# Optimization experiments

Measured on AMD Instinct MI355X. Metric: run time of the kernel, lower is better.

## Reference

```python
import jax, jax.numpy as jnp
import numpy as np

B, T, H, W = 4096, 15, 28, 28
F1, F3 = 500, 10
# conv1 firing threshold from the original: 15 * (28*28 / (5*5)) * 0.35 * 0.16
CONV1_T = 15.0 * (28.0 * 28.0 / 25.0) * 0.35 * 0.16  # = 26.3424


def setup_inputs() -> dict:
    key = jax.random.key(0)
    k_in, k_w1, k_w3 = jax.random.split(key, 3)
    # Intensity-to-latency cumulative spike encoding (SpykeTorch style):
    # a pixel with intensity u fires at timestep ~ (1-u)*T and stays on
    # (spike trains are cumulative over the time dimension).
    u = jax.random.uniform(k_in, (B, 1, 1, H, W))
    t = jnp.arange(T, dtype=jnp.float32).reshape(1, T, 1, 1, 1)
    inp = (u * T <= (t + 1.0)).astype(jnp.float32)  # [B,T,1,H,W], binary, cumulative in t
    # snn.Convolution initializes weights as N(mean=0.8, std=0.05)
    w1 = 0.8 + 0.05 * jax.random.normal(k_w1, (F1, 1, H, W), dtype=jnp.float32)
    w3 = 0.8 + 0.05 * jax.random.normal(k_w3, (F3, F1), dtype=jnp.float32)
    return {"input": inp, "w1": w1, "w3": w3, "max_layer": 3}


def reference(input, w1, w3, max_layer):
    # --- conv1: kernel spans the full 28x28 field -> output spatial dims 1x1,
    # so the convolution is exactly a per-timestep GEMM (spatial dims squeezed).
    pot1 = jnp.einsum('btchw,fchw->btf', input, w1)          # [B,T,F1]
    # sf.fire(pot, CONV1_T, True): zero sub-threshold potentials, spikes = sign
    thr1 = jnp.where(pot1 >= CONV1_T, pot1, 0.0)
    spk1 = jnp.sign(thr1)
    if max_layer == 1:
        return spk1, thr1

    # --- conv3: 1x1 conv 500 -> 10 (spatial dims remain 1x1)
    pot3 = jnp.einsum('btf,gf->btg', spk1, w3)               # [B,T,F3]
    # sf.fire(pot) with threshold=None: keep only the last timestep, spikes = sign
    last = (jnp.arange(T) == T - 1).astype(pot3.dtype)[None, :, None]
    spk3 = jnp.sign(pot3 * last)                             # [B,T,F3]

    # --- sf.get_k_winners(pot3, k=1, r=0, spk3), vectorized over batch:
    # earliest spike time per feature (T - #spikes, clamped to T-1)
    first_t = jnp.clip(T - spk3.sum(axis=1), 0, T - 1).astype(jnp.int32)  # [B,F3]
    vals = jnp.take_along_axis(pot3, first_t[:, None, :], axis=1)         # [B,1,F3]
    trunc = spk3 * vals                                                   # [B,T,F3]
    v = trunc.max(axis=(1, 2), keepdims=True) * T   # large earliness bonus factor
    trunc = trunc + spk3 * v
    total = trunc.sum(axis=1)                                             # [B,F3]
    win = jnp.argmax(total, axis=1).astype(jnp.int32)
    # if no spike at all, original returns -1; decision_map is identity over 10
    out_cls = jnp.where(total.max(axis=1) != 0.0, win, -1)                # [B]
    return spk1, thr1, pot3, out_cls
```

## Files before the change

kernel.cpp:

```cpp
#include <hip/hip_runtime.h>
#include <hip/hip_bf16.h>
#include <stdint.h>


typedef _Float16     f16x8 __attribute__((ext_vector_type(8)));
typedef float        f32x4 __attribute__((ext_vector_type(4)));
typedef unsigned int u32x4 __attribute__((ext_vector_type(4)));

typedef __attribute__((address_space(3))) char        lds_char_t;
typedef const __attribute__((address_space(1))) char  gbl_char_t;

#define GLL16(gsrc, ldst) \
  __builtin_amdgcn_global_load_lds((gbl_char_t*)(gsrc), (lds_char_t*)(ldst), 16, 0, 0)

#define CONV1_T 26.3424f
#define KDIM 784
#define F1   500

__global__ __launch_bounds__(256)
void k_t0(const float* __restrict__ inp, unsigned int* __restrict__ t0nib)
{
    const int gid = blockIdx.x * 256 + threadIdx.x;
    const int b   = gid / 100;
    const int p8  = gid % 100;
    if (p8 >= 98) { t0nib[gid] = 0xFFFFFFFFu; return; }

    const float* base = inp + (size_t)b * 11760 + p8 * 8;
    float cnt[8];
    #pragma unroll
    for (int e = 0; e < 8; ++e) cnt[e] = 0.f;
    #pragma unroll
    for (int t = 0; t < 15; ++t) {
        const f32x4 v0 = *(const f32x4*)(base + t * 784);
        const f32x4 v1 = *(const f32x4*)(base + t * 784 + 4);
        #pragma unroll
        for (int e = 0; e < 4; ++e) { cnt[e] += v0[e]; cnt[e + 4] += v1[e]; }
    }
    unsigned int d = 0;
    #pragma unroll
    for (int e = 0; e < 8; ++e) {
        const unsigned int t0 = 15u - (unsigned int)cnt[e];
        d |= (t0 & 15u) << (4 * e);
    }
    t0nib[gid] = d;
}

__device__ __forceinline__
f16x8 rebuild_a(unsigned int d, int t)
{
    u32x4 br;
    #pragma unroll
    for (int h = 0; h < 4; ++h) {
        const unsigned int n0 = (d >> (8 * h))     & 15u;
        const unsigned int n1 = (d >> (8 * h + 4)) & 15u;
        br[h] = (n0 <= (unsigned)t ? 0x3C00u     : 0u)
              | (n1 <= (unsigned)t ? 0x3C000000u : 0u);
    }
    return __builtin_bit_cast(f16x8, br);
}

__global__ __launch_bounds__(256)
void k_prep(const float* __restrict__ w1, float* __restrict__ scratch)
{
    const int c = blockIdx.x * 256 + threadIdx.x;
    const int tile  = c >> 11;
    const int chunk = c & 2047;
    const int nb   = tile / 25;
    const int ks   = tile % 25;
    const int part = chunk >> 10;
    const int nl   = (chunk & 1023) >> 2;
    const int slot = chunk & 3;
    const int j    = slot ^ ((nl >> 1) & 3);
    const int k0   = ks * 32 + j * 8;
    const int ng   = nb * 256 + nl;

    f16x8 v;
    #pragma unroll
    for (int e = 0; e < 8; ++e) {
        const int kk = k0 + e;
        const float val = (ng < F1 && kk < KDIM) ? w1[ng * KDIM + kk] : 0.f;
        const _Float16 h = (_Float16)val;
        v[e] = part ? (_Float16)(val - (float)h) : h;
    }
    *(f16x8*)((char*)scratch + (size_t)c * 16) = v;
}

__global__ __launch_bounds__(512, 4)
void k_conv1_t0(const unsigned char* __restrict__ t0nib,
                const float* __restrict__ bsplit,
                float* __restrict__ spk1, float* __restrict__ thr1)
{
    __shared__ _Float16 sA[2][128 * 32];
    __shared__ _Float16 sB[2][2 * 256 * 32];

    const int tid  = threadIdx.x;
    const int lane = tid & 63;
    const int wid  = tid >> 6;
    const int wm   = wid >> 2;
    const int wn   = wid & 3;
    const int lr   = lane & 15;
    const int kg   = lane >> 4;

    const int bx   = blockIdx.x;
    const int nb   = (bx >> 3) & 1;
    const int mblk = ((bx >> 4) << 3) | (bx & 7);
    const long long rowBase = (long long)mblk * 128;

    const int sm  = tid >> 2;
    const int sk8 = tid & 3;
    const int aWr = sm * 32 + (sk8 ^ ((sm >> 1) & 3)) * 8;
    const long long am = rowBase + sm;
    const int at = (int)(am % 15);
    const unsigned char* atp = t0nib + (am / 15) * 400 + sk8 * 4;

    const char* gBsrc = (const char*)bsplit + (size_t)(nb * 25) * 32768
                      + (size_t)wid * 4096 + (size_t)lane * 16;

    f32x4 acc[4][4];
    #pragma unroll
    for (int i = 0; i < 4; ++i)
        #pragma unroll
        for (int j = 0; j < 4; ++j) acc[i][j] = {0.f, 0.f, 0.f, 0.f};

    int aOff[4], bOff[4];
    #pragma unroll
    for (int fm = 0; fm < 4; ++fm) {
        const int r = wm * 64 + fm * 16 + lr;
        aOff[fm] = r * 32 + (kg ^ ((r >> 1) & 3)) * 8;
    }
    #pragma unroll
    for (int fn = 0; fn < 4; ++fn) {
        const int n = wn * 64 + fn * 16 + lr;
        bOff[fn] = n * 32 + (kg ^ ((n >> 1) & 3)) * 8;
    }

    {
        #pragma unroll
        for (int i = 0; i < 4; ++i)
            GLL16(gBsrc + i * 1024, (lds_char_t*)&sB[0][0] + wid * 4096 + i * 1024);
        const unsigned int d = *(const unsigned int*)(atp);
        *(f16x8*)&sA[0][aWr] = rebuild_a(d, at);
    }
    __syncthreads();

    for (int ks = 0; ks < 25; ++ks) {
        const int  cur = ks & 1;
        const bool pf  = (ks + 1 < 25);

        unsigned int dNext = 0;
        if (pf) {
            dNext = *(const unsigned int*)(atp + (ks + 1) * 16);
            const char*  src = gBsrc + (size_t)(ks + 1) * 32768;
            lds_char_t*  dst = (lds_char_t*)&sB[cur ^ 1][0] + wid * 4096;
            #pragma unroll
            for (int i = 0; i < 4; ++i)
                GLL16(src + i * 1024, dst + i * 1024);
        }

        const f16x8 a0 = *(const f16x8*)&sA[cur][aOff[0]];
        const f16x8 a1 = *(const f16x8*)&sA[cur][aOff[1]];
        const f16x8 a2 = *(const f16x8*)&sA[cur][aOff[2]];
        const f16x8 a3 = *(const f16x8*)&sA[cur][aOff[3]];
        #pragma unroll
        for (int fn = 0; fn < 4; ++fn) {
            const f16x8 bh = *(const f16x8*)&sB[cur][bOff[fn]];
            const f16x8 bl = *(const f16x8*)&sB[cur][8192 + bOff[fn]];
            acc[0][fn] = __builtin_amdgcn_mfma_f32_16x16x32_f16(a0, bh, acc[0][fn], 0, 0, 0);
            acc[0][fn] = __builtin_amdgcn_mfma_f32_16x16x32_f16(a0, bl, acc[0][fn], 0, 0, 0);
            acc[1][fn] = __builtin_amdgcn_mfma_f32_16x16x32_f16(a1, bh, acc[1][fn], 0, 0, 0);
            acc[1][fn] = __builtin_amdgcn_mfma_f32_16x16x32_f16(a1, bl, acc[1][fn], 0, 0, 0);
            acc[2][fn] = __builtin_amdgcn_mfma_f32_16x16x32_f16(a2, bh, acc[2][fn], 0, 0, 0);
            acc[2][fn] = __builtin_amdgcn_mfma_f32_16x16x32_f16(a2, bl, acc[2][fn], 0, 0, 0);
            acc[3][fn] = __builtin_amdgcn_mfma_f32_16x16x32_f16(a3, bh, acc[3][fn], 0, 0, 0);
            acc[3][fn] = __builtin_amdgcn_mfma_f32_16x16x32_f16(a3, bl, acc[3][fn], 0, 0, 0);
        }

        if (pf)
            *(f16x8*)&sA[cur ^ 1][aWr] = rebuild_a(dNext, at);
        __syncthreads();
    }

    #pragma unroll
    for (int fm = 0; fm < 4; ++fm) {
        #pragma unroll
        for (int fn = 0; fn < 4; ++fn) {
            const int ng = nb * 256 + wn * 64 + fn * 16 + lr;
            if (ng < F1) {
                #pragma unroll
                for (int r = 0; r < 4; ++r) {
                    const long long m = rowBase + wm * 64 + fm * 16 + kg * 4 + r;
                    const float p   = acc[fm][fn][r];
                    const bool fire = (p >= CONV1_T);
                    thr1[m * F1 + ng] = fire ? p : 0.f;
                    spk1[m * F1 + ng] = fire ? 1.f : 0.f;
                }
            }
        }
    }
}

__global__ __launch_bounds__(512, 4)
void k_conv1_f32(const float* __restrict__ inp, const float* __restrict__ bsplit,
                 float* __restrict__ spk1, float* __restrict__ thr1)
{
    __shared__ _Float16 sA[2][128 * 32];
    __shared__ _Float16 sB[2][2 * 256 * 32];

    const int tid  = threadIdx.x;
    const int lane = tid & 63;
    const int wid  = tid >> 6;
    const int wm   = wid >> 2;
    const int wn   = wid & 3;
    const int lr   = lane & 15;
    const int kg   = lane >> 4;

    const int bx   = blockIdx.x;
    const int nb   = (bx >> 3) & 1;
    const int mblk = ((bx >> 4) << 3) | (bx & 7);
    const long long rowBase = (long long)mblk * 128;

    const int sm  = tid >> 2;
    const int sk8 = tid & 3;
    const int aWr = sm * 32 + (sk8 ^ ((sm >> 1) & 3)) * 8;
    const float* gA = inp + (rowBase + sm) * KDIM + sk8 * 8;

    const char* gBsrc = (const char*)bsplit + (size_t)(nb * 25) * 32768
                      + (size_t)wid * 4096 + (size_t)lane * 16;

    f32x4 acc[4][4];
    #pragma unroll
    for (int i = 0; i < 4; ++i)
        #pragma unroll
        for (int j = 0; j < 4; ++j) acc[i][j] = {0.f, 0.f, 0.f, 0.f};

    int aOff[4], bOff[4];
    #pragma unroll
    for (int fm = 0; fm < 4; ++fm) {
        const int r = wm * 64 + fm * 16 + lr;
        aOff[fm] = r * 32 + (kg ^ ((r >> 1) & 3)) * 8;
    }
    #pragma unroll
    for (int fn = 0; fn < 4; ++fn) {
        const int n = wn * 64 + fn * 16 + lr;
        bOff[fn] = n * 32 + (kg ^ ((n >> 1) & 3)) * 8;
    }

    {
        const f32x4 x0 = *(const f32x4*)(gA);
        const f32x4 x1 = *(const f32x4*)(gA + 4);
        #pragma unroll
        for (int i = 0; i < 4; ++i)
            GLL16(gBsrc + i * 1024, (lds_char_t*)&sB[0][0] + wid * 4096 + i * 1024);
        f16x8 v;
        #pragma unroll
        for (int e = 0; e < 4; ++e) { v[e] = (_Float16)x0[e]; v[e + 4] = (_Float16)x1[e]; }
        *(f16x8*)&sA[0][aWr] = v;
    }
    __syncthreads();

    for (int ks = 0; ks < 25; ++ks) {
        const int  cur = ks & 1;
        const bool pf  = (ks + 1 < 25);

        f32x4 x0 = {0.f, 0.f, 0.f, 0.f}, x1 = {0.f, 0.f, 0.f, 0.f};
        bool av = false;
        if (pf) {
            const int k0 = (ks + 1) * 32 + sk8 * 8;
            av = (k0 + 8 <= KDIM);
            if (av) {
                x0 = *(const f32x4*)(gA + (ks + 1) * 32);
                x1 = *(const f32x4*)(gA + (ks + 1) * 32 + 4);
            }
            const char*  src = gBsrc + (size_t)(ks + 1) * 32768;
            lds_char_t*  dst = (lds_char_t*)&sB[cur ^ 1][0] + wid * 4096;
            #pragma unroll
            for (int i = 0; i < 4; ++i)
                GLL16(src + i * 1024, dst + i * 1024);
        }

        const f16x8 a0 = *(const f16x8*)&sA[cur][aOff[0]];
        const f16x8 a1 = *(const f16x8*)&sA[cur][aOff[1]];
        const f16x8 a2 = *(const f16x8*)&sA[cur][aOff[2]];
        const f16x8 a3 = *(const f16x8*)&sA[cur][aOff[3]];
        #pragma unroll
        for (int fn = 0; fn < 4; ++fn) {
            const f16x8 bh = *(const f16x8*)&sB[cur][bOff[fn]];
            const f16x8 bl = *(const f16x8*)&sB[cur][8192 + bOff[fn]];
            acc[0][fn] = __builtin_amdgcn_mfma_f32_16x16x32_f16(a0, bh, acc[0][fn], 0, 0, 0);
            acc[0][fn] = __builtin_amdgcn_mfma_f32_16x16x32_f16(a0, bl, acc[0][fn], 0, 0, 0);
            acc[1][fn] = __builtin_amdgcn_mfma_f32_16x16x32_f16(a1, bh, acc[1][fn], 0, 0, 0);
            acc[1][fn] = __builtin_amdgcn_mfma_f32_16x16x32_f16(a1, bl, acc[1][fn], 0, 0, 0);
            acc[2][fn] = __builtin_amdgcn_mfma_f32_16x16x32_f16(a2, bh, acc[2][fn], 0, 0, 0);
            acc[2][fn] = __builtin_amdgcn_mfma_f32_16x16x32_f16(a2, bl, acc[2][fn], 0, 0, 0);
            acc[3][fn] = __builtin_amdgcn_mfma_f32_16x16x32_f16(a3, bh, acc[3][fn], 0, 0, 0);
            acc[3][fn] = __builtin_amdgcn_mfma_f32_16x16x32_f16(a3, bl, acc[3][fn], 0, 0, 0);
        }

        if (pf) {
            f16x8 v;
            #pragma unroll
            for (int e = 0; e < 4; ++e) {
                v[e]     = av ? (_Float16)x0[e] : (_Float16)0.f;
                v[e + 4] = av ? (_Float16)x1[e] : (_Float16)0.f;
            }
            *(f16x8*)&sA[cur ^ 1][aWr] = v;
        }
        __syncthreads();
    }

    #pragma unroll
    for (int fm = 0; fm < 4; ++fm) {
        #pragma unroll
        for (int fn = 0; fn < 4; ++fn) {
            const int ng = nb * 256 + wn * 64 + fn * 16 + lr;
            if (ng < F1) {
                #pragma unroll
                for (int r = 0; r < 4; ++r) {
                    const long long m = rowBase + wm * 64 + fm * 16 + kg * 4 + r;
                    const float p   = acc[fm][fn][r];
                    const bool fire = (p >= CONV1_T);
                    thr1[m * F1 + ng] = fire ? p : 0.f;
                    spk1[m * F1 + ng] = fire ? 1.f : 0.f;
                }
            }
        }
    }
}

__global__ __launch_bounds__(256)
void k_conv3(const float* __restrict__ spk1, const float* __restrict__ w3,
             float* __restrict__ pot3)
{
    const int tid  = threadIdx.x;
    const int lane = tid & 63;
    const int wid  = tid >> 6;
    const int gw   = blockIdx.x * 4 + wid;
    const long long row0 = (long long)gw * 16;
    const int lr = lane & 15;
    const int kg = lane >> 4;
    const int n  = (lr < 10) ? lr : 0;

    const float* arow = spk1 + (row0 + lr) * F1;
    const float* brow = w3 + (size_t)n * F1;

    f32x4 acc = {0.f, 0.f, 0.f, 0.f};
    #pragma unroll
    for (int ks = 0; ks < 16; ++ks) {
        const int k0 = ks * 32 + kg * 8;
        f16x8 a, b;
        if (k0 + 8 <= F1) {
            const f32x4 a0 = *(const f32x4*)(arow + k0);
            const f32x4 a1 = *(const f32x4*)(arow + k0 + 4);
            const f32x4 b0 = *(const f32x4*)(brow + k0);
            const f32x4 b1 = *(const f32x4*)(brow + k0 + 4);
            #pragma unroll
            for (int e = 0; e < 4; ++e) {
                a[e] = (_Float16)a0[e]; a[e + 4] = (_Float16)a1[e];
                b[e] = (_Float16)b0[e]; b[e + 4] = (_Float16)b1[e];
            }
        } else {
            #pragma unroll
            for (int e = 0; e < 8; ++e) {
                const int k = k0 + e;
                a[e] = (k < F1) ? (_Float16)arow[k] : (_Float16)0.f;
                b[e] = (k < F1) ? (_Float16)brow[k] : (_Float16)0.f;
            }
        }
        acc = __builtin_amdgcn_mfma_f32_16x16x32_f16(a, b, acc, 0, 0, 0);
    }
    if (lr < 10) {
        #pragma unroll
        for (int r = 0; r < 4; ++r) {
            const long long m = row0 + kg * 4 + r;
            pot3[m * 10 + lr] = acc[r];
        }
    }
}

__global__ __launch_bounds__(256)
void k_winner(const float* __restrict__ pot3, float* __restrict__ outCls, int nB)
{
    const int b = blockIdx.x * 256 + threadIdx.x;
    if (b >= nB) return;
    const float* p = pot3 + (long long)b * 150 + 140;

    float pv[10], s[10];
    float mv = 0.f;
    #pragma unroll
    for (int g = 0; g < 10; ++g) {
        const float v = p[g];
        pv[g] = v;
        s[g]  = (v > 0.f) ? 1.f : ((v < 0.f) ? -1.f : 0.f);
        mv = fmaxf(mv, s[g] * v);
    }
    const float vbig = mv * 15.f;
    float bm = -INFINITY; int bi = 0;
    #pragma unroll
    for (int g = 0; g < 10; ++g) {
        const float tot = s[g] * pv[g] + s[g] * vbig;
        if (tot > bm) { bm = tot; bi = g; }
    }
    outCls[b] = (bm != 0.f) ? (float)bi : -1.f;
}

extern "C" void kernel_launch(void* const* d_in, const int* in_sizes, int n_in,
                              void* d_out, int out_size, void* d_ws, size_t ws_size,
                              hipStream_t stream)
{
    const float* inp = (const float*)d_in[0];
    const float* w1  = (const float*)d_in[1];
    const float* w3  = (const float*)d_in[2];

    float* out  = (float*)d_out;
    float* spk1 = out;
    float* thr1 = out + 30720000LL;
    float* pot3 = out + 61440000LL;
    float* cls  = out + 62054400LL;

    if (ws_size >= 3276800) {
        float*        w1split = (float*)d_ws;
        unsigned int* t0nib   = (unsigned int*)((char*)d_ws + 1638400);
        k_prep    <<<400,  256, 0, stream>>>(w1, w1split);
        k_t0      <<<1600, 256, 0, stream>>>(inp, t0nib);
        k_conv1_t0<<<960,  512, 0, stream>>>((const unsigned char*)t0nib, w1split,
                                             spk1, thr1);
    } else {
        float* scratch = pot3;
        k_prep     <<<400, 256, 0, stream>>>(w1, scratch);
        k_conv1_f32<<<960, 512, 0, stream>>>(inp, scratch, spk1, thr1);
    }
    k_conv3 <<<960, 256, 0, stream>>>(spk1, w3, pot3);
    k_winner<<<16,  256, 0, stream>>>(pot3, cls, 4096);
}
```

Measured before the change: 205.8 us.

## Use single fp16 weight GEMM with exact fp32 recompute near threshold

Drops the hi/lo fp16 split of w1, so the conv1 GEMM issues half the MFMAs and loads half the B tile into LDS. Accumulators whose value falls within a small delta of the firing threshold are recomputed exactly in fp32 against the original weights, which keeps spike decisions correct. Values not near the threshold still carry fp16 weight rounding in thr1, a precision risk. The rare serial fallback dot product may also cause divergence stalls.

```diff
diff --git a/kernel.cpp b/kernel.cpp
--- a/kernel.cpp
+++ b/kernel.cpp
@@ -13,7 +13,8 @@
 #define GLL16(gsrc, ldst) \
   __builtin_amdgcn_global_load_lds((gbl_char_t*)(gsrc), (lds_char_t*)(ldst), 16, 0, 0)
 
-#define CONV1_T 26.3424f
+#define CONV1_T   26.3424f
+#define FIX_DELTA 0.05f
 #define KDIM 784
 #define F1   500
 
@@ -59,16 +60,48 @@
     return __builtin_bit_cast(f16x8, br);
 }
 
+__device__ __attribute__((noinline))
+float fix_dot_t0(const unsigned char* __restrict__ nib,
+                 const float* __restrict__ w, int t)
+{
+    float s0 = 0.f, s1 = 0.f, s2 = 0.f, s3 = 0.f;
+    for (int k = 0; k < KDIM; k += 4) {
+        const unsigned int b0 = nib[k >> 1];
+        const unsigned int b1 = nib[(k >> 1) + 1];
+        const float a0 = ((int)(b0 & 15u) <= t) ? 1.f : 0.f;
+        const float a1 = ((int)(b0 >> 4)  <= t) ? 1.f : 0.f;
+        const float a2 = ((int)(b1 & 15u) <= t) ? 1.f : 0.f;
+        const float a3 = ((int)(b1 >> 4)  <= t) ? 1.f : 0.f;
+        s0 = fmaf(a0, w[k],     s0);
+        s1 = fmaf(a1, w[k + 1], s1);
+        s2 = fmaf(a2, w[k + 2], s2);
+        s3 = fmaf(a3, w[k + 3], s3);
+    }
+    return (s0 + s1) + (s2 + s3);
+}
+
+__device__ __attribute__((noinline))
+float fix_dot(const float* __restrict__ a, const float* __restrict__ w)
+{
+    float s0 = 0.f, s1 = 0.f, s2 = 0.f, s3 = 0.f;
+    for (int k = 0; k < KDIM; k += 4) {
+        s0 = fmaf(a[k],     w[k],     s0);
+        s1 = fmaf(a[k + 1], w[k + 1], s1);
+        s2 = fmaf(a[k + 2], w[k + 2], s2);
+        s3 = fmaf(a[k + 3], w[k + 3], s3);
+    }
+    return (s0 + s1) + (s2 + s3);
+}
+
 __global__ __launch_bounds__(256)
 void k_prep(const float* __restrict__ w1, float* __restrict__ scratch)
 {
     const int c = blockIdx.x * 256 + threadIdx.x;
-    const int tile  = c >> 11;
-    const int chunk = c & 2047;
+    const int tile  = c >> 10;
+    const int chunk = c & 1023;
     const int nb   = tile / 25;
     const int ks   = tile % 25;
-    const int part = chunk >> 10;
-    const int nl   = (chunk & 1023) >> 2;
+    const int nl   = chunk >> 2;
     const int slot = chunk & 3;
     const int j    = slot ^ ((nl >> 1) & 3);
     const int k0   = ks * 32 + j * 8;
@@ -78,9 +111,7 @@
     #pragma unroll
     for (int e = 0; e < 8; ++e) {
         const int kk = k0 + e;
-        const float val = (ng < F1 && kk < KDIM) ? w1[ng * KDIM + kk] : 0.f;
-        const _Float16 h = (_Float16)val;
-        v[e] = part ? (_Float16)(val - (float)h) : h;
+        v[e] = (ng < F1 && kk < KDIM) ? (_Float16)w1[ng * KDIM + kk] : (_Float16)0.f;
     }
     *(f16x8*)((char*)scratch + (size_t)c * 16) = v;
 }
@@ -88,10 +119,11 @@
 __global__ __launch_bounds__(512, 4)
 void k_conv1_t0(const unsigned char* __restrict__ t0nib,
                 const float* __restrict__ bsplit,
+                const float* __restrict__ w1,
                 float* __restrict__ spk1, float* __restrict__ thr1)
 {
     __shared__ _Float16 sA[2][128 * 32];
-    __shared__ _Float16 sB[2][2 * 256 * 32];
+    __shared__ _Float16 sB[2][256 * 32];
 
     const int tid  = threadIdx.x;
     const int lane = tid & 63;
@@ -113,8 +145,8 @@
     const int at = (int)(am % 15);
     const unsigned char* atp = t0nib + (am / 15) * 400 + sk8 * 4;
 
-    const char* gBsrc = (const char*)bsplit + (size_t)(nb * 25) * 32768
-                      + (size_t)wid * 4096 + (size_t)lane * 16;
+    const char* gBsrc = (const char*)bsplit + (size_t)(nb * 25) * 16384
+                      + (size_t)wid * 2048 + (size_t)lane * 16;
 
     f32x4 acc[4][4];
     #pragma unroll
@@ -136,8 +168,8 @@
 
     {
         #pragma unroll
-        for (int i = 0; i < 4; ++i)
-            GLL16(gBsrc + i * 1024, (lds_char_t*)&sB[0][0] + wid * 4096 + i * 1024);
+        for (int i = 0; i < 2; ++i)
+            GLL16(gBsrc + i * 1024, (lds_char_t*)&sB[0][0] + wid * 2048 + i * 1024);
         const unsigned int d = *(const unsigned int*)(atp);
         *(f16x8*)&sA[0][aWr] = rebuild_a(d, at);
     }
@@ -150,10 +182,10 @@
         unsigned int dNext = 0;
         if (pf) {
             dNext = *(const unsigned int*)(atp + (ks + 1) * 16);
-            const char*  src = gBsrc + (size_t)(ks + 1) * 32768;
-            lds_char_t*  dst = (lds_char_t*)&sB[cur ^ 1][0] + wid * 4096;
+            const char*  src = gBsrc + (size_t)(ks + 1) * 16384;
+            lds_char_t*  dst = (lds_char_t*)&sB[cur ^ 1][0] + wid * 2048;
             #pragma unroll
-            for (int i = 0; i < 4; ++i)
+            for (int i = 0; i < 2; ++i)
                 GLL16(src + i * 1024, dst + i * 1024);
         }
 
@@ -163,16 +195,11 @@
         const f16x8 a3 = *(const f16x8*)&sA[cur][aOff[3]];
         #pragma unroll
         for (int fn = 0; fn < 4; ++fn) {
-            const f16x8 bh = *(const f16x8*)&sB[cur][bOff[fn]];
-            const f16x8 bl = *(const f16x8*)&sB[cur][8192 + bOff[fn]];
-            acc[0][fn] = __builtin_amdgcn_mfma_f32_16x16x32_f16(a0, bh, acc[0][fn], 0, 0, 0);
-            acc[0][fn] = __builtin_amdgcn_mfma_f32_16x16x32_f16(a0, bl, acc[0][fn], 0, 0, 0);
-            acc[1][fn] = __builtin_amdgcn_mfma_f32_16x16x32_f16(a1, bh, acc[1][fn], 0, 0, 0);
-            acc[1][fn] = __builtin_amdgcn_mfma_f32_16x16x32_f16(a1, bl, acc[1][fn], 0, 0, 0);
-            acc[2][fn] = __builtin_amdgcn_mfma_f32_16x16x32_f16(a2, bh, acc[2][fn], 0, 0, 0);
-            acc[2][fn] = __builtin_amdgcn_mfma_f32_16x16x32_f16(a2, bl, acc[2][fn], 0, 0, 0);
-            acc[3][fn] = __builtin_amdgcn_mfma_f32_16x16x32_f16(a3, bh, acc[3][fn], 0, 0, 0);
-            acc[3][fn] = __builtin_amdgcn_mfma_f32_16x16x32_f16(a3, bl, acc[3][fn], 0, 0, 0);
+            const f16x8 b = *(const f16x8*)&sB[cur][bOff[fn]];
+            acc[0][fn] = __builtin_amdgcn_mfma_f32_16x16x32_f16(a0, b, acc[0][fn], 0, 0, 0);
+            acc[1][fn] = __builtin_amdgcn_mfma_f32_16x16x32_f16(a1, b, acc[1][fn], 0, 0, 0);
+            acc[2][fn] = __builtin_amdgcn_mfma_f32_16x16x32_f16(a2, b, acc[2][fn], 0, 0, 0);
+            acc[3][fn] = __builtin_amdgcn_mfma_f32_16x16x32_f16(a3, b, acc[3][fn], 0, 0, 0);
         }
 
         if (pf)
@@ -189,7 +216,10 @@
                 #pragma unroll
                 for (int r = 0; r < 4; ++r) {
                     const long long m = rowBase + wm * 64 + fm * 16 + kg * 4 + r;
-                    const float p   = acc[fm][fn][r];
+                    float p = acc[fm][fn][r];
+                    if (__builtin_expect(fabsf(p - CONV1_T) < FIX_DELTA, 0))
+                        p = fix_dot_t0(t0nib + (m / 15) * 400,
+                                       w1 + (size_t)ng * KDIM, (int)(m % 15));
                     const bool fire = (p >= CONV1_T);
                     thr1[m * F1 + ng] = fire ? p : 0.f;
                     spk1[m * F1 + ng] = fire ? 1.f : 0.f;
@@ -201,10 +231,11 @@
 
 __global__ __launch_bounds__(512, 4)
 void k_conv1_f32(const float* __restrict__ inp, const float* __restrict__ bsplit,
+                 const float* __restrict__ w1,
                  float* __restrict__ spk1, float* __restrict__ thr1)
 {
     __shared__ _Float16 sA[2][128 * 32];
-    __shared__ _Float16 sB[2][2 * 256 * 32];
+    __shared__ _Float16 sB[2][256 * 32];
 
     const int tid  = threadIdx.x;
     const int lane = tid & 63;
@@ -224,8 +255,8 @@
     const int aWr = sm * 32 + (sk8 ^ ((sm >> 1) & 3)) * 8;
     const float* gA = inp + (rowBase + sm) * KDIM + sk8 * 8;
 
-    const char* gBsrc = (const char*)bsplit + (size_t)(nb * 25) * 32768
-                      + (size_t)wid * 4096 + (size_t)lane * 16;
+    const char* gBsrc = (const char*)bsplit + (size_t)(nb * 25) * 16384
+                      + (size_t)wid * 2048 + (size_t)lane * 16;
 
     f32x4 acc[4][4];
     #pragma unroll
@@ -249,8 +280,8 @@
         const f32x4 x0 = *(const f32x4*)(gA);
         const f32x4 x1 = *(const f32x4*)(gA + 4);
         #pragma unroll
-        for (int i = 0; i < 4; ++i)
-            GLL16(gBsrc + i * 1024, (lds_char_t*)&sB[0][0] + wid * 4096 + i * 1024);
+        for (int i = 0; i < 2; ++i)
+            GLL16(gBsrc + i * 1024, (lds_char_t*)&sB[0][0] + wid * 2048 + i * 1024);
         f16x8 v;
         #pragma unroll
         for (int e = 0; e < 4; ++e) { v[e] = (_Float16)x0[e]; v[e + 4] = (_Float16)x1[e]; }
@@ -271,10 +302,10 @@
                 x0 = *(const f32x4*)(gA + (ks + 1) * 32);
                 x1 = *(const f32x4*)(gA + (ks + 1) * 32 + 4);
             }
-            const char*  src = gBsrc + (size_t)(ks + 1) * 32768;
-            lds_char_t*  dst = (lds_char_t*)&sB[cur ^ 1][0] + wid * 4096;
+            const char*  src = gBsrc + (size_t)(ks + 1) * 16384;
+            lds_char_t*  dst = (lds_char_t*)&sB[cur ^ 1][0] + wid * 2048;
             #pragma unroll
-            for (int i = 0; i < 4; ++i)
+            for (int i = 0; i < 2; ++i)
                 GLL16(src + i * 1024, dst + i * 1024);
         }
 
@@ -284,16 +315,11 @@
         const f16x8 a3 = *(const f16x8*)&sA[cur][aOff[3]];
         #pragma unroll
         for (int fn = 0; fn < 4; ++fn) {
-            const f16x8 bh = *(const f16x8*)&sB[cur][bOff[fn]];
-            const f16x8 bl = *(const f16x8*)&sB[cur][8192 + bOff[fn]];
-            acc[0][fn] = __builtin_amdgcn_mfma_f32_16x16x32_f16(a0, bh, acc[0][fn], 0, 0, 0);
-            acc[0][fn] = __builtin_amdgcn_mfma_f32_16x16x32_f16(a0, bl, acc[0][fn], 0, 0, 0);
-            acc[1][fn] = __builtin_amdgcn_mfma_f32_16x16x32_f16(a1, bh, acc[1][fn], 0, 0, 0);
-            acc[1][fn] = __builtin_amdgcn_mfma_f32_16x16x32_f16(a1, bl, acc[1][fn], 0, 0, 0);
-            acc[2][fn] = __builtin_amdgcn_mfma_f32_16x16x32_f16(a2, bh, acc[2][fn], 0, 0, 0);
-            acc[2][fn] = __builtin_amdgcn_mfma_f32_16x16x32_f16(a2, bl, acc[2][fn], 0, 0, 0);
-            acc[3][fn] = __builtin_amdgcn_mfma_f32_16x16x32_f16(a3, bh, acc[3][fn], 0, 0, 0);
-            acc[3][fn] = __builtin_amdgcn_mfma_f32_16x16x32_f16(a3, bl, acc[3][fn], 0, 0, 0);
+            const f16x8 b = *(const f16x8*)&sB[cur][bOff[fn]];
+            acc[0][fn] = __builtin_amdgcn_mfma_f32_16x16x32_f16(a0, b, acc[0][fn], 0, 0, 0);
+            acc[1][fn] = __builtin_amdgcn_mfma_f32_16x16x32_f16(a1, b, acc[1][fn], 0, 0, 0);
+            acc[2][fn] = __builtin_amdgcn_mfma_f32_16x16x32_f16(a2, b, acc[2][fn], 0, 0, 0);
+            acc[3][fn] = __builtin_amdgcn_mfma_f32_16x16x32_f16(a3, b, acc[3][fn], 0, 0, 0);
         }
 
         if (pf) {
@@ -317,7 +343,9 @@
                 #pragma unroll
                 for (int r = 0; r < 4; ++r) {
                     const long long m = rowBase + wm * 64 + fm * 16 + kg * 4 + r;
-                    const float p   = acc[fm][fn][r];
+                    float p = acc[fm][fn][r];
+                    if (__builtin_expect(fabsf(p - CONV1_T) < FIX_DELTA, 0))
+                        p = fix_dot(inp + m * KDIM, w1 + (size_t)ng * KDIM);
                     const bool fire = (p >= CONV1_T);
                     thr1[m * F1 + ng] = fire ? p : 0.f;
                     spk1[m * F1 + ng] = fire ? 1.f : 0.f;
@@ -417,17 +445,17 @@
     float* pot3 = out + 61440000LL;
     float* cls  = out + 62054400LL;
 
-    if (ws_size >= 3276800) {
-        float*        w1split = (float*)d_ws;
-        unsigned int* t0nib   = (unsigned int*)((char*)d_ws + 1638400);
-        k_prep    <<<400,  256, 0, stream>>>(w1, w1split);
+    if (ws_size >= 2457600) {
+        float*        w1f16 = (float*)d_ws;
+        unsigned int* t0nib = (unsigned int*)((char*)d_ws + 819200);
+        k_prep    <<<200,  256, 0, stream>>>(w1, w1f16);
         k_t0      <<<1600, 256, 0, stream>>>(inp, t0nib);
-        k_conv1_t0<<<960,  512, 0, stream>>>((const unsigned char*)t0nib, w1split,
-                                             spk1, thr1);
+        k_conv1_t0<<<960,  512, 0, stream>>>((const unsigned char*)t0nib, w1f16,
+                                             w1, spk1, thr1);
     } else {
         float* scratch = pot3;
-        k_prep     <<<400, 256, 0, stream>>>(w1, scratch);
-        k_conv1_f32<<<960, 512, 0, stream>>>(inp, scratch, spk1, thr1);
+        k_prep     <<<200, 256, 0, stream>>>(w1, scratch);
+        k_conv1_f32<<<960, 512, 0, stream>>>(inp, scratch, w1, spk1, thr1);
     }
     k_conv3 <<<960, 256, 0, stream>>>(spk1, w3, pot3);
     k_winner<<<16,  256, 0, stream>>>(pot3, cls, 4096);
```

After: 311.1 us. +51.2%, slower.

## Fuse conv3 into conv1 epilogue using LDS spike tile and atomic accumulation

Applied to the files above, without the earlier changes.

The conv1 kernel now writes its binary spike tile as fp16 into shared memory and immediately runs the 500->10 conv3 GEMM with MFMA on it. Each of the two N-halves adds its partial result into pot3 with atomicAdd. A zero-fill kernel clears pot3 first, and the separate conv3 pass, which re-read the full spk1 array from global memory, is dropped on the default path. The cost is extra LDS use (80KB), fp16 rounding of w3, atomic traffic, and an extra small launch.

```diff
diff --git a/kernel.cpp b/kernel.cpp
--- a/kernel.cpp
+++ b/kernel.cpp
@@ -43,6 +43,13 @@
         d |= (t0 & 15u) << (4 * e);
     }
     t0nib[gid] = d;
+}
+
+__global__ __launch_bounds__(256)
+void k_zero(float* __restrict__ p, int n)
+{
+    const int i = blockIdx.x * 256 + threadIdx.x;
+    if (i < n) p[i] = 0.f;
 }
 
 __device__ __forceinline__
@@ -88,10 +95,13 @@
 __global__ __launch_bounds__(512, 4)
 void k_conv1_t0(const unsigned char* __restrict__ t0nib,
                 const float* __restrict__ bsplit,
-                float* __restrict__ spk1, float* __restrict__ thr1)
-{
-    __shared__ _Float16 sA[2][128 * 32];
-    __shared__ _Float16 sB[2][2 * 256 * 32];
+                const float* __restrict__ w3,
+                float* __restrict__ spk1, float* __restrict__ thr1,
+                float* __restrict__ pot3)
+{
+    __shared__ char smem[81920];
+    _Float16* sAh = (_Float16*)smem;
+    _Float16* sBh = (_Float16*)(smem + 16384);
 
     const int tid  = threadIdx.x;
     const int lane = tid & 63;
@@ -137,9 +147,10 @@
     {
         #pragma unroll
         for (int i = 0; i < 4; ++i)
-            GLL16(gBsrc + i * 1024, (lds_char_t*)&sB[0][0] + wid * 4096 + i * 1024);
+            GLL16(gBsrc + i * 1024,
+                  (lds_char_t*)smem + 16384 + (size_t)wid * 4096 + i * 1024);
         const unsigned int d = *(const unsigned int*)(atp);
-        *(f16x8*)&sA[0][aWr] = rebuild_a(d, at);
+        *(f16x8*)&sAh[aWr] = rebuild_a(d, at);
     }
     __syncthreads();
 
@@ -150,6 +161,166 @@
         unsigned int dNext = 0;
         if (pf) {
             dNext = *(const unsigned int*)(atp + (ks + 1) * 16);
+            const char*  src = gBsrc + (size_t)(ks + 1) * 32768;
+            lds_char_t*  dst = (lds_char_t*)smem + 16384 + (size_t)(cur ^ 1) * 32768
+                             + (size_t)wid * 4096;
+            #pragma unroll
+            for (int i = 0; i < 4; ++i)
+                GLL16(src + i * 1024, dst + i * 1024);
+        }
+
+        const _Float16* sAc = sAh + (size_t)cur * 4096;
+        const _Float16* sBc = sBh + (size_t)cur * 16384;
+        const f16x8 a0 = *(const f16x8*)&sAc[aOff[0]];
+        const f16x8 a1 = *(const f16x8*)&sAc[aOff[1]];
+        const f16x8 a2 = *(const f16x8*)&sAc[aOff[2]];
+        const f16x8 a3 = *(const f16x8*)&sAc[aOff[3]];
+        #pragma unroll
+        for (int fn = 0; fn < 4; ++fn) {
+            const f16x8 bh = *(const f16x8*)&sBc[bOff[fn]];
+            const f16x8 bl = *(const f16x8*)&sBc[8192 + bOff[fn]];
+            acc[0][fn] = __builtin_amdgcn_mfma_f32_16x16x32_f16(a0, bh, acc[0][fn], 0, 0, 0);
+            acc[0][fn] = __builtin_amdgcn_mfma_f32_16x16x32_f16(a0, bl, acc[0][fn], 0, 0, 0);
+            acc[1][fn] = __builtin_amdgcn_mfma_f32_16x16x32_f16(a1, bh, acc[1][fn], 0, 0, 0);
+            acc[1][fn] = __builtin_amdgcn_mfma_f32_16x16x32_f16(a1, bl, acc[1][fn], 0, 0, 0);
+            acc[2][fn] = __builtin_amdgcn_mfma_f32_16x16x32_f16(a2, bh, acc[2][fn], 0, 0, 0);
+            acc[2][fn] = __builtin_amdgcn_mfma_f32_16x16x32_f16(a2, bl, acc[2][fn], 0, 0, 0);
+            acc[3][fn] = __builtin_amdgcn_mfma_f32_16x16x32_f16(a3, bh, acc[3][fn], 0, 0, 0);
+            acc[3][fn] = __builtin_amdgcn_mfma_f32_16x16x32_f16(a3, bl, acc[3][fn], 0, 0, 0);
+        }
+
+        if (pf)
+            *(f16x8*)&sAh[(size_t)(cur ^ 1) * 4096 + aWr] = rebuild_a(dNext, at);
+        __syncthreads();
+    }
+
+    #pragma unroll
+    for (int fm = 0; fm < 4; ++fm) {
+        #pragma unroll
+        for (int fn = 0; fn < 4; ++fn) {
+            const int colL = wn * 64 + fn * 16 + lr;
+            const int ng   = nb * 256 + colL;
+            #pragma unroll
+            for (int r = 0; r < 4; ++r) {
+                const int rowL = wm * 64 + fm * 16 + kg * 4 + r;
+                const long long m = rowBase + rowL;
+                const float p   = acc[fm][fn][r];
+                const bool fire = (p >= CONV1_T);
+                int sbyte = rowL * 512 + colL * 2;
+                sbyte ^= ((rowL & 7) << 4);
+                *(_Float16*)(smem + sbyte) = fire ? (_Float16)1.f : (_Float16)0.f;
+                if (ng < F1) {
+                    thr1[m * F1 + ng] = fire ? p : 0.f;
+                    spk1[m * F1 + ng] = fire ? 1.f : 0.f;
+                }
+            }
+        }
+    }
+    __syncthreads();
+
+    {
+        f32x4 acc3 = {0.f, 0.f, 0.f, 0.f};
+        const int mrow = wid * 16 + lr;
+        #pragma unroll
+        for (int kc = 0; kc < 8; ++kc) {
+            int abyte = mrow * 512 + (kc * 32 + kg * 8) * 2;
+            abyte ^= ((mrow & 7) << 4);
+            const f16x8 a3 = *(const f16x8*)(smem + abyte);
+            f16x8 b3;
+            const int f0 = nb * 256 + kc * 32 + kg * 8;
+            if (lr < 10) {
+                const float* wr = w3 + lr * F1 + f0;
+                #pragma unroll
+                for (int e = 0; e < 8; ++e)
+                    b3[e] = (f0 + e < F1) ? (_Float16)wr[e] : (_Float16)0.f;
+            } else {
+                #pragma unroll
+                for (int e = 0; e < 8; ++e) b3[e] = (_Float16)0.f;
+            }
+            acc3 = __builtin_amdgcn_mfma_f32_16x16x32_f16(a3, b3, acc3, 0, 0, 0);
+        }
+        if (lr < 10) {
+            #pragma unroll
+            for (int r = 0; r < 4; ++r) {
+                const long long m = rowBase + wid * 16 + kg * 4 + r;
+                atomicAdd(&pot3[m * 10 + lr], acc3[r]);
+            }
+        }
+    }
+}
+
+__global__ __launch_bounds__(512, 4)
+void k_conv1_f32(const float* __restrict__ inp, const float* __restrict__ bsplit,
+                 float* __restrict__ spk1, float* __restrict__ thr1)
+{
+    __shared__ _Float16 sA[2][128 * 32];
+    __shared__ _Float16 sB[2][2 * 256 * 32];
+
+    const int tid  = threadIdx.x;
+    const int lane = tid & 63;
+    const int wid  = tid >> 6;
+    const int wm   = wid >> 2;
+    const int wn   = wid & 3;
+    const int lr   = lane & 15;
+    const int kg   = lane >> 4;
+
+    const int bx   = blockIdx.x;
+    const int nb   = (bx >> 3) & 1;
+    const int mblk = ((bx >> 4) << 3) | (bx & 7);
+    const long long rowBase = (long long)mblk * 128;
+
+    const int sm  = tid >> 2;
+    const int sk8 = tid & 3;
+    const int aWr = sm * 32 + (sk8 ^ ((sm >> 1) & 3)) * 8;
+    const float* gA = inp + (rowBase + sm) * KDIM + sk8 * 8;
+
+    const char* gBsrc = (const char*)bsplit + (size_t)(nb * 25) * 32768
+                      + (size_t)wid * 4096 + (size_t)lane * 16;
+
+    f32x4 acc[4][4];
+    #pragma unroll
+    for (int i = 0; i < 4; ++i)
+        #pragma unroll
+        for (int j = 0; j < 4; ++j) acc[i][j] = {0.f, 0.f, 0.f, 0.f};
+
+    int aOff[4], bOff[4];
+    #pragma unroll
+    for (int fm = 0; fm < 4; ++fm) {
+        const int r = wm * 64 + fm * 16 + lr;
+        aOff[fm] = r * 32 + (kg ^ ((r >> 1) & 3)) * 8;
+    }
+    #pragma unroll
+    for (int fn = 0; fn < 4; ++fn) {
+        const int n = wn * 64 + fn * 16 + lr;
+        bOff[fn] = n * 32 + (kg ^ ((n >> 1) & 3)) * 8;
+    }
+
+    {
+        const f32x4 x0 = *(const f32x4*)(gA);
+        const f32x4 x1 = *(const f32x4*)(gA + 4);
+        #pragma unroll
+        for (int i = 0; i < 4; ++i)
+            GLL16(gBsrc + i * 1024, (lds_char_t*)&sB[0][0] + wid * 4096 + i * 1024);
+        f16x8 v;
+        #pragma unroll
+        for (int e = 0; e < 4; ++e) { v[e] = (_Float16)x0[e]; v[e + 4] = (_Float16)x1[e]; }
+        *(f16x8*)&sA[0][aWr] = v;
+    }
+    __syncthreads();
+
+    for (int ks = 0; ks < 25; ++ks) {
+        const int  cur = ks & 1;
+        const bool pf  = (ks + 1 < 25);
+
+        f32x4 x0 = {0.f, 0.f, 0.f, 0.f}, x1 = {0.f, 0.f, 0.f, 0.f};
+        bool av = false;
+        if (pf) {
+            const int k0 = (ks + 1) * 32 + sk8 * 8;
+            av = (k0 + 8 <= KDIM);
+            if (av) {
+                x0 = *(const f32x4*)(gA + (ks + 1) * 32);
+                x1 = *(const f32x4*)(gA + (ks + 1) * 32 + 4);
+            }
             const char*  src = gBsrc + (size_t)(ks + 1) * 32768;
             lds_char_t*  dst = (lds_char_t*)&sB[cur ^ 1][0] + wid * 4096;
             #pragma unroll
@@ -175,8 +346,15 @@
             acc[3][fn] = __builtin_amdgcn_mfma_f32_16x16x32_f16(a3, bl, acc[3][fn], 0, 0, 0);
         }
 
-        if (pf)
-            *(f16x8*)&sA[cur ^ 1][aWr] = rebuild_a(dNext, at);
+        if (pf) {
+            f16x8 v;
+            #pragma unroll
+            for (int e = 0; e < 4; ++e) {
+                v[e]     = av ? (_Float16)x0[e] : (_Float16)0.f;
+                v[e + 4] = av ? (_Float16)x1[e] : (_Float16)0.f;
+            }
+            *(f16x8*)&sA[cur ^ 1][aWr] = v;
+        }
         __syncthreads();
     }
 
@@ -199,134 +377,6 @@
     }
 }
 
-__global__ __launch_bounds__(512, 4)
-void k_conv1_f32(const float* __restrict__ inp, const float* __restrict__ bsplit,
-                 float* __restrict__ spk1, float* __restrict__ thr1)
-{
-    __shared__ _Float16 sA[2][128 * 32];
-    __shared__ _Float16 sB[2][2 * 256 * 32];
-
-    const int tid  = threadIdx.x;
-    const int lane = tid & 63;
-    const int wid  = tid >> 6;
-    const int wm   = wid >> 2;
-    const int wn   = wid & 3;
-    const int lr   = lane & 15;
-    const int kg   = lane >> 4;
-
-    const int bx   = blockIdx.x;
-    const int nb   = (bx >> 3) & 1;
-    const int mblk = ((bx >> 4) << 3) | (bx & 7);
-    const long long rowBase = (long long)mblk * 128;
-
-    const int sm  = tid >> 2;
-    const int sk8 = tid & 3;
-    const int aWr = sm * 32 + (sk8 ^ ((sm >> 1) & 3)) * 8;
-    const float* gA = inp + (rowBase + sm) * KDIM + sk8 * 8;
-
-    const char* gBsrc = (const char*)bsplit + (size_t)(nb * 25) * 32768
-                      + (size_t)wid * 4096 + (size_t)lane * 16;
-
-    f32x4 acc[4][4];
-    #pragma unroll
-    for (int i = 0; i < 4; ++i)
-        #pragma unroll
-        for (int j = 0; j < 4; ++j) acc[i][j] = {0.f, 0.f, 0.f, 0.f};
-
-    int aOff[4], bOff[4];
-    #pragma unroll
-    for (int fm = 0; fm < 4; ++fm) {
-        const int r = wm * 64 + fm * 16 + lr;
-        aOff[fm] = r * 32 + (kg ^ ((r >> 1) & 3)) * 8;
-    }
-    #pragma unroll
-    for (int fn = 0; fn < 4; ++fn) {
-        const int n = wn * 64 + fn * 16 + lr;
-        bOff[fn] = n * 32 + (kg ^ ((n >> 1) & 3)) * 8;
-    }
-
-    {
-        const f32x4 x0 = *(const f32x4*)(gA);
-        const f32x4 x1 = *(const f32x4*)(gA + 4);
-        #pragma unroll
-        for (int i = 0; i < 4; ++i)
-            GLL16(gBsrc + i * 1024, (lds_char_t*)&sB[0][0] + wid * 4096 + i * 1024);
-        f16x8 v;
-        #pragma unroll
-        for (int e = 0; e < 4; ++e) { v[e] = (_Float16)x0[e]; v[e + 4] = (_Float16)x1[e]; }
-        *(f16x8*)&sA[0][aWr] = v;
-    }
-    __syncthreads();
-
-    for (int ks = 0; ks < 25; ++ks) {
-        const int  cur = ks & 1;
-        const bool pf  = (ks + 1 < 25);
-
-        f32x4 x0 = {0.f, 0.f, 0.f, 0.f}, x1 = {0.f, 0.f, 0.f, 0.f};
-        bool av = false;
-        if (pf) {
-            const int k0 = (ks + 1) * 32 + sk8 * 8;
-            av = (k0 + 8 <= KDIM);
-            if (av) {
-                x0 = *(const f32x4*)(gA + (ks + 1) * 32);
-                x1 = *(const f32x4*)(gA + (ks + 1) * 32 + 4);
-            }
-            const char*  src = gBsrc + (size_t)(ks + 1) * 32768;
-            lds_char_t*  dst = (lds_char_t*)&sB[cur ^ 1][0] + wid * 4096;
-            #pragma unroll
-            for (int i = 0; i < 4; ++i)
-                GLL16(src + i * 1024, dst + i * 1024);
-        }
-
-        const f16x8 a0 = *(const f16x8*)&sA[cur][aOff[0]];
-        const f16x8 a1 = *(const f16x8*)&sA[cur][aOff[1]];
-        const f16x8 a2 = *(const f16x8*)&sA[cur][aOff[2]];
-        const f16x8 a3 = *(const f16x8*)&sA[cur][aOff[3]];
-        #pragma unroll
-        for (int fn = 0; fn < 4; ++fn) {
-            const f16x8 bh = *(const f16x8*)&sB[cur][bOff[fn]];
-            const f16x8 bl = *(const f16x8*)&sB[cur][8192 + bOff[fn]];
-            acc[0][fn] = __builtin_amdgcn_mfma_f32_16x16x32_f16(a0, bh, acc[0][fn], 0, 0, 0);
-            acc[0][fn] = __builtin_amdgcn_mfma_f32_16x16x32_f16(a0, bl, acc[0][fn], 0, 0, 0);
-            acc[1][fn] = __builtin_amdgcn_mfma_f32_16x16x32_f16(a1, bh, acc[1][fn], 0, 0, 0);
-            acc[1][fn] = __builtin_amdgcn_mfma_f32_16x16x32_f16(a1, bl, acc[1][fn], 0, 0, 0);
-            acc[2][fn] = __builtin_amdgcn_mfma_f32_16x16x32_f16(a2, bh, acc[2][fn], 0, 0, 0);
-            acc[2][fn] = __builtin_amdgcn_mfma_f32_16x16x32_f16(a2, bl, acc[2][fn], 0, 0, 0);
-            acc[3][fn] = __builtin_amdgcn_mfma_f32_16x16x32_f16(a3, bh, acc[3][fn], 0, 0, 0);
-            acc[3][fn] = __builtin_amdgcn_mfma_f32_16x16x32_f16(a3, bl, acc[3][fn], 0, 0, 0);
-        }
-
-        if (pf) {
-            f16x8 v;
-            #pragma unroll
-            for (int e = 0; e < 4; ++e) {
-                v[e]     = av ? (_Float16)x0[e] : (_Float16)0.f;
-                v[e + 4] = av ? (_Float16)x1[e] : (_Float16)0.f;
-            }
-            *(f16x8*)&sA[cur ^ 1][aWr] = v;
-        }
-        __syncthreads();
-    }
-
-    #pragma unroll
-    for (int fm = 0; fm < 4; ++fm) {
-        #pragma unroll
-        for (int fn = 0; fn < 4; ++fn) {
-            const int ng = nb * 256 + wn * 64 + fn * 16 + lr;
-            if (ng < F1) {
-                #pragma unroll
-                for (int r = 0; r < 4; ++r) {
-                    const long long m = rowBase + wm * 64 + fm * 16 + kg * 4 + r;
-                    const float p   = acc[fm][fn][r];
-                    const bool fire = (p >= CONV1_T);
-                    thr1[m * F1 + ng] = fire ? p : 0.f;
-                    spk1[m * F1 + ng] = fire ? 1.f : 0.f;
-                }
-            }
-        }
-    }
-}
-
 __global__ __launch_bounds__(256)
 void k_conv3(const float* __restrict__ spk1, const float* __restrict__ w3,
              float* __restrict__ pot3)
@@ -422,13 +472,14 @@
         unsigned int* t0nib   = (unsigned int*)((char*)d_ws + 1638400);
         k_prep    <<<400,  256, 0, stream>>>(w1, w1split);
         k_t0      <<<1600, 256, 0, stream>>>(inp, t0nib);
+        k_zero    <<<2400, 256, 0, stream>>>(pot3, 614400);
         k_conv1_t0<<<960,  512, 0, stream>>>((const unsigned char*)t0nib, w1split,
-                                             spk1, thr1);
+                                             w3, spk1, thr1, pot3);
     } else {
         float* scratch = pot3;
         k_prep     <<<400, 256, 0, stream>>>(w1, scratch);
         k_conv1_f32<<<960, 512, 0, stream>>>(inp, scratch, spk1, thr1);
-    }
-    k_conv3 <<<960, 256, 0, stream>>>(spk1, w3, pot3);
-    k_winner<<<16,  256, 0, stream>>>(pot3, cls, 4096);
-}
+        k_conv3    <<<960, 256, 0, stream>>>(spk1, w3, pot3);
+    }
+    k_winner<<<16, 256, 0, stream>>>(pot3, cls, 4096);
+}
```

Measured after the change: 187.6 us. 1.1x faster.
